# Kernel optimization log

Measured on AMD Instinct MI355X. Metric: run time of the kernel, lower is better.

The kernel has to match this reference:

```python
import jax, jax.numpy as jnp
import numpy as np

TREE_DEPTH = 4
N_LEAVES = 2 ** TREE_DEPTH      # 16
N_INTERNAL = 2 ** TREE_DEPTH - 1  # 15
TEMP = 1.0
EPS = 1e-5


def _build_paths(depth):
    nl = 2 ** depth
    pi = np.zeros((nl, depth), np.int32)
    pd = np.zeros((nl, depth), np.float32)
    for leaf in range(nl):
        node = 0
        for d in range(depth):
            pi[leaf, d] = node
            bit = (leaf >> (depth - 1 - d)) & 1
            pd[leaf, d] = 1.0 - bit
            node = 2 * node + 1 + bit
    return jnp.asarray(pi), jnp.asarray(pd)

PATH_IDX, PATH_DIR = _build_paths(TREE_DEPTH)


def setup_inputs() -> dict:
    key = jax.random.key(0)
    k0, k1, k2, k3 = jax.random.split(key, 4)
    B, S, D, O, T = 4, 2048, 1024, 512, 16
    x = jax.random.normal(k0, (B, S, D), jnp.float32)
    decision_weights = 0.1 * jax.random.normal(k1, (T, N_INTERNAL, D), jnp.float32)
    decision_biases = jnp.zeros((T, N_INTERNAL), jnp.float32)
    xavier = float(np.sqrt(2.0 / (N_LEAVES + O)))
    leaf_outputs = xavier * jax.random.normal(k2, (T, N_LEAVES, O), jnp.float32)
    gate_w = 0.02 * jax.random.normal(k3, (D, T), jnp.float32)
    gate_b = jnp.zeros((T,), jnp.float32)
    node_temp_logits = jnp.zeros((T, N_INTERNAL), jnp.float32)
    ln_gamma = jnp.ones((O,), jnp.float32)
    ln_beta = jnp.zeros((O,), jnp.float32)
    return dict(x=x, decision_weights=decision_weights, decision_biases=decision_biases,
                leaf_outputs=leaf_outputs, gate_w=gate_w, gate_b=gate_b,
                node_temp_logits=node_temp_logits, ln_gamma=ln_gamma, ln_beta=ln_beta)


def reference(x, decision_weights, decision_biases, leaf_outputs,
              gate_w, gate_b, node_temp_logits, ln_gamma, ln_beta):
    # decision logits: (B,S,T,N)
    logits = jnp.einsum('bsd,tnd->bstn', x, decision_weights) + decision_biases
    # per-node learnable temperature (softplus(0.5413) ~= 1)
    node_temps = TEMP * jax.nn.softplus(node_temp_logits + 0.5413)
    decisions = jax.nn.sigmoid(logits / node_temps)
    # gather decisions along each root->leaf path: (B,S,T,L,depth)
    relevant = decisions[..., PATH_IDX]
    probs_per_level = PATH_DIR * relevant + (1.0 - PATH_DIR) * (1.0 - relevant)
    leaf_probs = jnp.prod(probs_per_level, axis=-1)  # (B,S,T,L)
    per_tree = jnp.einsum('bstl,tlo->bsto', leaf_probs, leaf_outputs)
    gate = jax.nn.softmax(x @ gate_w + gate_b, axis=-1)  # (B,S,T)
    out = jnp.einsum('bsto,bst->bso', per_tree, gate)
    # LayerNorm over last dim
    mu = jnp.mean(out, axis=-1, keepdims=True)
    var = jnp.var(out, axis=-1, keepdims=True)
    return (out - mu) / jnp.sqrt(var + EPS) * ln_gamma + ln_beta
```

## Files before the change

kernel.cpp:

```cpp
#include <hip/hip_runtime.h>
#include <math.h>

#define TOK 8192
#define DD  1024
#define OO  512
#define NC  256

#define WC4_HI 0
#define WC4_LO (512*1024)
#define LO4_HI (1024*1024)
#define LO4_LO (1280*1024)
#define PAR_B  (1536*1024)

typedef __attribute__((ext_vector_type(8))) short short8;
typedef __attribute__((ext_vector_type(4))) float f32x4;

#define MFMA16(a,b,c) __builtin_amdgcn_mfma_f32_16x16x32_bf16((a),(b),(c),0,0,0)

__device__ __forceinline__ ushort f2bh(float f) {
  union { float f; unsigned u; } v; v.f = f;
  unsigned r = v.u + 0x7fffu + ((v.u >> 16) & 1u);
  return (ushort)(r >> 16);
}
__device__ __forceinline__ float bh2f(ushort h) {
  union { unsigned u; float f; } v; v.u = ((unsigned)h) << 16; return v.f;
}
__device__ __forceinline__ void split2(float f, ushort& h, ushort& l) {
  h = f2bh(f);
  l = f2bh(f - bh2f(h));
}

__global__ __launch_bounds__(256) void k_prep(
    const float* __restrict__ dw, const float* __restrict__ db,
    const float* __restrict__ lo_in, const float* __restrict__ gw,
    const float* __restrict__ ntl, char* __restrict__ ws) {
  const int bid = blockIdx.x, tid = threadIdx.x;
  if (bid < 16) {
    __shared__ char pt[65536];
    const int n0 = (bid & 3) * 64;
    const int k0 = (bid >> 2) * 256;
    const int kl4 = (tid & 63) << 2;
#pragma unroll
    for (int i = 0; i < 16; ++i) {
      const int row = (tid >> 6) + 4 * i;
      const int n = n0 + row;
      float v[4];
      if (n < 240) {
        const float4 t4 = *(const float4*)&dw[(size_t)n * DD + k0 + kl4];
        v[0] = t4.x; v[1] = t4.y; v[2] = t4.z; v[3] = t4.w;
      } else {
        const int t = n - 240;
#pragma unroll
        for (int c = 0; c < 4; ++c) v[c] = gw[(size_t)(k0 + kl4 + c) * 16 + t];
      }
      ushort4 h, l;
      split2(v[0], h.x, l.x); split2(v[1], h.y, l.y);
      split2(v[2], h.z, l.z); split2(v[3], h.w, l.w);
      const int u = kl4 >> 3, half = (kl4 >> 2) & 1;
      const int boff = row * 512 + ((u ^ (row & 31)) << 4) + half * 8;
      *(ushort4*)(pt + boff) = h;
      *(ushort4*)(pt + 32768 + boff) = l;
    }
    __syncthreads();
#pragma unroll
    for (int j = 0; j < 8; ++j) {
      const int u = tid + 256 * j;
      const int c = u & 63;
      const int kk = u >> 6;
      const int src = c * 512 + ((kk ^ (c & 31)) << 4);
      const size_t dst = ((size_t)((k0 >> 3) + kk) * 256 + n0 + c) * 16;
      *(short8*)(ws + WC4_HI + dst) = *(const short8*)(pt + src);
      *(short8*)(ws + WC4_LO + dst) = *(const short8*)(pt + 32768 + src);
    }
  } else if (bid < 80) {
    const int idx  = (bid - 16) * 256 + tid;
    const int k8   = idx >> 9;
    const int ocol = idx & 511;
    float v[8];
#pragma unroll
    for (int c = 0; c < 8; ++c) v[c] = lo_in[(size_t)(k8 * 8 + c) * OO + ocol];
    short8 h, l;
#pragma unroll
    for (int e = 0; e < 8; ++e) {
      ushort hh, ll; split2(v[e], hh, ll);
      h[e] = (short)hh; l[e] = (short)ll;
    }
    const size_t o16 = ((size_t)k8 * 512 + ocol) * 16;
    *(short8*)(ws + LO4_HI + o16) = h;
    *(short8*)(ws + LO4_LO + o16) = l;
  } else {
    if (tid < 240) {
      float v = ntl[tid] + 0.5413f;
      float sp = (v > 20.f) ? v : log1pf(expf(v));
      float* par = (float*)(ws + PAR_B);
      par[tid]       = db[tid];
      par[240 + tid] = 1.0f / sp;
    }
  }
}

#define XSB(b)  ((b) * 16384)
#define WF_HI   32768
#define WF_LO   49152
#define SM_SZ   65536

__global__ __launch_bounds__(512) void k_fused(
    const float* __restrict__ x, const char* __restrict__ ws,
    const float* __restrict__ gate_b, const float* __restrict__ gamma,
    const float* __restrict__ beta, float* __restrict__ out) {
  __shared__ __align__(16) char sm[SM_SZ];

  const char* wc4_hi = ws + WC4_HI;
  const char* wc4_lo = ws + WC4_LO;
  const char* lo4_hi = ws + LO4_HI;
  const char* lo4_lo = ws + LO4_LO;
  const float* par   = (const float*)(ws + PAR_B);

  const int tid  = threadIdx.x;
  const int wv   = tid >> 6;
  const int lane = tid & 63;
  const int l15  = lane & 15;
  const int kgrp = lane >> 4;
  const int m0   = blockIdx.x * 32;

  f32x4 acc00 = {0,0,0,0}, acc01 = {0,0,0,0}, acc10 = {0,0,0,0}, acc11 = {0,0,0,0};
  short8 ah0, ah1, al0, al1;
  short8 b1h[4][2], b1l[4][2];
  float4 pxa, pxb;

  auto xload = [&](int CH) {
    const int m_ = tid >> 5, kl = (tid & 31) << 2;
    pxa = *(const float4*)&x[(size_t)(m0 + m_) * DD + CH * 128 + kl];
    pxb = *(const float4*)&x[(size_t)(m0 + 16 + m_) * DD + CH * 128 + kl];
  };
  auto xstore = [&](int BUF) {
    const int kl2 = ((tid & 31) << 2) * 2;
    ushort4 h, l;
    split2(pxa.x, h.x, l.x); split2(pxa.y, h.y, l.y);
    split2(pxa.z, h.z, l.z); split2(pxa.w, h.w, l.w);
    {
      const int m_ = tid >> 5;
      const int off = (m_ * 256 + kl2) ^ ((m_ & 15) << 4);
      *(ushort4*)(sm + XSB(BUF) + off) = h;
      *(ushort4*)(sm + XSB(BUF) + 8192 + off) = l;
    }
    split2(pxb.x, h.x, l.x); split2(pxb.y, h.y, l.y);
    split2(pxb.z, h.z, l.z); split2(pxb.w, h.w, l.w);
    {
      const int m_ = 16 + (tid >> 5);
      const int off = (m_ * 256 + kl2) ^ ((m_ & 15) << 4);
      *(ushort4*)(sm + XSB(BUF) + off) = h;
      *(ushort4*)(sm + XSB(BUF) + 8192 + off) = l;
    }
  };
#define LOADB1(F, S) do {                                               \
    const int Fc = (F) < 31 ? (F) : 31;                                 \
    const size_t base = ((size_t)(Fc * 4 + kgrp) * 256) * 16;           \
    _Pragma("unroll")                                                   \
    for (int j = 0; j < 2; ++j) {                                       \
      const size_t o = base + (size_t)(wv * 32 + j * 16 + l15) * 16;    \
      b1h[S][j] = *(const short8*)(wc4_hi + o);                         \
      b1l[S][j] = *(const short8*)(wc4_lo + o);                         \
    }                                                                   \
  } while (0)
  auto afrag = [&](int CB, int KS) {
    const int k0 = KS * 64 + kgrp * 16;
    const int a0 = (l15 * 256 + k0) ^ ((l15 & 15) << 4);
    const int a1 = ((16 + l15) * 256 + k0) ^ ((l15 & 15) << 4);
    ah0 = *(const short8*)(sm + XSB(CB) + a0);
    al0 = *(const short8*)(sm + XSB(CB) + 8192 + a0);
    ah1 = *(const short8*)(sm + XSB(CB) + a1);
    al1 = *(const short8*)(sm + XSB(CB) + 8192 + a1);
  };
#define MFMASTEP(S) do {                                                   \
    acc00 = MFMA16(ah0, b1h[S][0], acc00); acc00 = MFMA16(ah0, b1l[S][0], acc00); \
    acc00 = MFMA16(al0, b1h[S][0], acc00);                                 \
    acc01 = MFMA16(ah0, b1h[S][1], acc01); acc01 = MFMA16(ah0, b1l[S][1], acc01); \
    acc01 = MFMA16(al0, b1h[S][1], acc01);                                 \
    acc10 = MFMA16(ah1, b1h[S][0], acc10); acc10 = MFMA16(ah1, b1l[S][0], acc10); \
    acc10 = MFMA16(al1, b1h[S][0], acc10);                                 \
    acc11 = MFMA16(ah1, b1h[S][1], acc11); acc11 = MFMA16(ah1, b1l[S][1], acc11); \
    acc11 = MFMA16(al1, b1h[S][1], acc11);                                 \
  } while (0)

  xload(0);
  xstore(0);
  LOADB1(0, 0);
  LOADB1(1, 1);

  for (int ch = 0; ch < 8; ++ch) {
    __syncthreads();
    const int cb = ch & 1;
    if (ch < 7) xload(ch + 1);
    const int f = ch * 4;
    LOADB1(f + 2, 2); afrag(cb, 0); MFMASTEP(0);
    LOADB1(f + 3, 3); afrag(cb, 1); MFMASTEP(1);
    LOADB1(f + 4, 0); afrag(cb, 2); MFMASTEP(2);
    LOADB1(f + 5, 1); afrag(cb, 3); MFMASTEP(3);
    if (ch < 7) xstore(cb ^ 1);
  }
  __syncthreads();

  {
    float* actp = (float*)sm;
    const f32x4 a[2][2] = {{acc00, acc01}, {acc10, acc11}};
#pragma unroll
    for (int mi = 0; mi < 2; ++mi)
#pragma unroll
      for (int j = 0; j < 2; ++j)
#pragma unroll
        for (int r = 0; r < 4; ++r) {
          const int row = mi * 16 + kgrp * 4 + r;
          const int col = wv * 32 + j * 16 + l15;
          actp[row * 256 + col] = a[mi][j][r];
        }
  }
  __syncthreads();

  short8 c2h[3][4], c2l[3][4];
#define LOADB2(F, S) do {                                               \
    const size_t base = ((size_t)((F) * 4 + kgrp) * 512) * 16;          \
    _Pragma("unroll")                                                   \
    for (int t = 0; t < 4; ++t) {                                       \
      const size_t o = base + (size_t)(wv * 64 + t * 16 + l15) * 16;    \
      c2h[S][t] = *(const short8*)(lo4_hi + o);                         \
      c2l[S][t] = *(const short8*)(lo4_lo + o);                         \
    }                                                                   \
  } while (0)
  LOADB2(0, 0);

  {
    const float* actp = (const float*)sm;
    const int token = tid >> 4;
    const int tr    = tid & 15;
    const float* arow_p = actp + token * 256;

    float dec[15];
#pragma unroll
    for (int i = 0; i < 15; ++i) {
      const int ci = tr * 15 + i;
      const float z = (arow_p[ci] + par[ci]) * par[240 + ci];
      dec[i] = 1.f / (1.f + expf(-z));
    }
    float gl = arow_p[240 + tr] + gate_b[tr];
    float gmax = gl;
#pragma unroll
    for (int msk = 8; msk >= 1; msk >>= 1) gmax = fmaxf(gmax, __shfl_xor(gmax, msk, 16));
    const float ge = expf(gl - gmax);
    float gsum = ge;
#pragma unroll
    for (int msk = 8; msk >= 1; msk >>= 1) gsum += __shfl_xor(gsum, msk, 16);
    const float gate = ge / gsum;

    float lp[16];
#pragma unroll
    for (int l = 0; l < 16; ++l) {
      float p = gate;
      int node = 0;
#pragma unroll
      for (int d = 0; d < 4; ++d) {
        const int bit = (l >> (3 - d)) & 1;
        p *= bit ? (1.f - dec[node]) : dec[node];
        node = 2 * node + 1 + bit;
      }
      lp[l] = p;
    }
    short8 h0, h1, l0, l1;
#pragma unroll
    for (int e = 0; e < 8; ++e) {
      ushort hh, ll;
      split2(lp[e], hh, ll);     h0[e] = (short)hh; l0[e] = (short)ll;
      split2(lp[8 + e], hh, ll); h1[e] = (short)hh; l1[e] = (short)ll;
    }
    const int b0 = (token * 512 + tr * 32) ^ ((token & 15) << 4);
    const int b1 = (token * 512 + tr * 32 + 16) ^ ((token & 15) << 4);
    *(short8*)(sm + WF_HI + b0) = h0;
    *(short8*)(sm + WF_HI + b1) = h1;
    *(short8*)(sm + WF_LO + b0) = l0;
    *(short8*)(sm + WF_LO + b1) = l1;
  }
  __syncthreads();

  f32x4 ac0[4], ac1[4];
#pragma unroll
  for (int t = 0; t < 4; ++t) { ac0[t] = (f32x4){0,0,0,0}; ac1[t] = (f32x4){0,0,0,0}; }
  short8 wah0, wah1, wal0, wal1;
  auto wafrag = [&](int FC) {
    const int k0 = FC * 64 + kgrp * 16;
    const int a0 = (l15 * 512 + k0) ^ ((l15 & 15) << 4);
    const int a1 = ((16 + l15) * 512 + k0) ^ ((l15 & 15) << 4);
    wah0 = *(const short8*)(sm + WF_HI + a0);
    wal0 = *(const short8*)(sm + WF_LO + a0);
    wah1 = *(const short8*)(sm + WF_HI + a1);
    wal1 = *(const short8*)(sm + WF_LO + a1);
  };
#define MFMA2STEP(S) do {                                                  \
    _Pragma("unroll")                                                      \
    for (int t = 0; t < 4; ++t) {                                          \
      ac0[t] = MFMA16(wah0, c2h[S][t], ac0[t]);                            \
      ac0[t] = MFMA16(wah0, c2l[S][t], ac0[t]);                            \
      ac0[t] = MFMA16(wal0, c2h[S][t], ac0[t]);                            \
      ac1[t] = MFMA16(wah1, c2h[S][t], ac1[t]);                            \
      ac1[t] = MFMA16(wah1, c2l[S][t], ac1[t]);                            \
      ac1[t] = MFMA16(wal1, c2h[S][t], ac1[t]);                            \
    }                                                                      \
  } while (0)

  LOADB2(1, 1);
  LOADB2(2, 2); wafrag(0); MFMA2STEP(0);
  LOADB2(3, 0); wafrag(1); MFMA2STEP(1);
  LOADB2(4, 1); wafrag(2); MFMA2STEP(2);
  LOADB2(5, 2); wafrag(3); MFMA2STEP(0);
  LOADB2(6, 0); wafrag(4); MFMA2STEP(1);
  LOADB2(7, 1); wafrag(5); MFMA2STEP(2);
  wafrag(6); MFMA2STEP(0);
  wafrag(7); MFMA2STEP(1);

  float* ps = (float*)sm;
#pragma unroll
  for (int mi = 0; mi < 2; ++mi)
#pragma unroll
    for (int r = 0; r < 4; ++r) {
      float s = 0.f, q = 0.f;
#pragma unroll
      for (int t = 0; t < 4; ++t) {
        const float v = (mi == 0) ? ac0[t][r] : ac1[t][r];
        s += v; q += v * v;
      }
#pragma unroll
      for (int msk = 8; msk >= 1; msk >>= 1) {
        s += __shfl_xor(s, msk, 16);
        q += __shfl_xor(q, msk, 16);
      }
      if (l15 == 0) {
        const int row = mi * 16 + kgrp * 4 + r;
        ps[(row * 8 + wv) * 2 + 0] = s;
        ps[(row * 8 + wv) * 2 + 1] = q;
      }
    }
  __syncthreads();

#pragma unroll
  for (int mi = 0; mi < 2; ++mi)
#pragma unroll
    for (int r = 0; r < 4; ++r) {
      const int row = mi * 16 + kgrp * 4 + r;
      float S = 0.f, Q = 0.f;
#pragma unroll
      for (int p = 0; p < 8; ++p) {
        S += ps[(row * 8 + p) * 2 + 0];
        Q += ps[(row * 8 + p) * 2 + 1];
      }
      const float mu  = S * (1.f / 512.f);
      const float var = Q * (1.f / 512.f) - mu * mu;
      const float rs  = rsqrtf(var + 1e-5f);
#pragma unroll
      for (int t = 0; t < 4; ++t) {
        const int col = wv * 64 + t * 16 + l15;
        const float v = (mi == 0) ? ac0[t][r] : ac1[t][r];
        out[(size_t)(m0 + row) * OO + col] = (v - mu) * rs * gamma[col] + beta[col];
      }
    }
}

extern "C" void kernel_launch(void* const* d_in, const int* in_sizes, int n_in,
                              void* d_out, int out_size, void* d_ws, size_t ws_size,
                              hipStream_t stream) {
  const float* x   = (const float*)d_in[0];
  const float* dw  = (const float*)d_in[1];
  const float* db  = (const float*)d_in[2];
  const float* lo  = (const float*)d_in[3];
  const float* gw  = (const float*)d_in[4];
  const float* gb  = (const float*)d_in[5];
  const float* ntl = (const float*)d_in[6];
  const float* g   = (const float*)d_in[7];
  const float* b   = (const float*)d_in[8];
  char* ws   = (char*)d_ws;
  float* out = (float*)d_out;

  k_prep<<<81, 256, 0, stream>>>(dw, db, lo, gw, ntl, ws);
  k_fused<<<256, 512, 0, stream>>>(x, ws, gb, g, b, out);
}
```

Measured before the change: 124.3 us.

## Double block size to 1024 threads, splitting output columns across 16 waves

Raises the fused kernel's block from 512 to 1024 threads, so 16 waves each own half as many output columns in both GEMM stages. Per-thread accumulators, weight fragments and x loads are halved. The leaf-probability stage is restricted to the first 512 threads, and the LayerNorm partial reduction now spans 16 waves. The goal is more latency hiding per CU with only 256 blocks, at the cost of more A-fragment LDS reads per wave, an idle half-block in the decision stage, and tighter register limits under the 1024 launch bound.

```diff
diff --git a/kernel.cpp b/kernel.cpp
--- a/kernel.cpp
+++ b/kernel.cpp
@@ -104,7 +104,7 @@
 #define WF_LO   49152
 #define SM_SZ   65536
 
-__global__ __launch_bounds__(512) void k_fused(
+__global__ __launch_bounds__(1024) void k_fused(
     const float* __restrict__ x, const char* __restrict__ ws,
     const float* __restrict__ gate_b, const float* __restrict__ gamma,
     const float* __restrict__ beta, float* __restrict__ out) {
@@ -123,64 +123,47 @@
   const int kgrp = lane >> 4;
   const int m0   = blockIdx.x * 32;
 
-  f32x4 acc00 = {0,0,0,0}, acc01 = {0,0,0,0}, acc10 = {0,0,0,0}, acc11 = {0,0,0,0};
+  f32x4 acc00 = {0,0,0,0}, acc10 = {0,0,0,0};
   short8 ah0, ah1, al0, al1;
-  short8 b1h[4][2], b1l[4][2];
-  float4 pxa, pxb;
+  short8 b1h[4], b1l[4];
+  float4 px;
+
+  const int xm = tid >> 5;
+  const int xk = (tid & 31) << 2;
 
   auto xload = [&](int CH) {
-    const int m_ = tid >> 5, kl = (tid & 31) << 2;
-    pxa = *(const float4*)&x[(size_t)(m0 + m_) * DD + CH * 128 + kl];
-    pxb = *(const float4*)&x[(size_t)(m0 + 16 + m_) * DD + CH * 128 + kl];
+    px = *(const float4*)&x[(size_t)(m0 + xm) * DD + CH * 128 + xk];
   };
   auto xstore = [&](int BUF) {
-    const int kl2 = ((tid & 31) << 2) * 2;
     ushort4 h, l;
-    split2(pxa.x, h.x, l.x); split2(pxa.y, h.y, l.y);
-    split2(pxa.z, h.z, l.z); split2(pxa.w, h.w, l.w);
-    {
-      const int m_ = tid >> 5;
-      const int off = (m_ * 256 + kl2) ^ ((m_ & 15) << 4);
-      *(ushort4*)(sm + XSB(BUF) + off) = h;
-      *(ushort4*)(sm + XSB(BUF) + 8192 + off) = l;
-    }
-    split2(pxb.x, h.x, l.x); split2(pxb.y, h.y, l.y);
-    split2(pxb.z, h.z, l.z); split2(pxb.w, h.w, l.w);
-    {
-      const int m_ = 16 + (tid >> 5);
-      const int off = (m_ * 256 + kl2) ^ ((m_ & 15) << 4);
-      *(ushort4*)(sm + XSB(BUF) + off) = h;
-      *(ushort4*)(sm + XSB(BUF) + 8192 + off) = l;
-    }
+    split2(px.x, h.x, l.x); split2(px.y, h.y, l.y);
+    split2(px.z, h.z, l.z); split2(px.w, h.w, l.w);
+    const int off = (xm * 256 + xk * 2) ^ ((xm & 15) << 4);
+    *(ushort4*)(sm + XSB(BUF) + off) = h;
+    *(ushort4*)(sm + XSB(BUF) + 8192 + off) = l;
   };
 #define LOADB1(F, S) do {                                               \
     const int Fc = (F) < 31 ? (F) : 31;                                 \
-    const size_t base = ((size_t)(Fc * 4 + kgrp) * 256) * 16;           \
-    _Pragma("unroll")                                                   \
-    for (int j = 0; j < 2; ++j) {                                       \
-      const size_t o = base + (size_t)(wv * 32 + j * 16 + l15) * 16;    \
-      b1h[S][j] = *(const short8*)(wc4_hi + o);                         \
-      b1l[S][j] = *(const short8*)(wc4_lo + o);                         \
-    }                                                                   \
+    const size_t o = ((size_t)(Fc * 4 + kgrp) * 256 + wv * 16 + l15) * 16; \
+    b1h[S] = *(const short8*)(wc4_hi + o);                              \
+    b1l[S] = *(const short8*)(wc4_lo + o);                              \
   } while (0)
   auto afrag = [&](int CB, int KS) {
     const int k0 = KS * 64 + kgrp * 16;
-    const int a0 = (l15 * 256 + k0) ^ ((l15 & 15) << 4);
-    const int a1 = ((16 + l15) * 256 + k0) ^ ((l15 & 15) << 4);
+    const int a0 = (l15 * 256 + k0) ^ (l15 << 4);
+    const int a1 = ((16 + l15) * 256 + k0) ^ (l15 << 4);
     ah0 = *(const short8*)(sm + XSB(CB) + a0);
     al0 = *(const short8*)(sm + XSB(CB) + 8192 + a0);
     ah1 = *(const short8*)(sm + XSB(CB) + a1);
     al1 = *(const short8*)(sm + XSB(CB) + 8192 + a1);
   };
-#define MFMASTEP(S) do {                                                   \
-    acc00 = MFMA16(ah0, b1h[S][0], acc00); acc00 = MFMA16(ah0, b1l[S][0], acc00); \
-    acc00 = MFMA16(al0, b1h[S][0], acc00);                                 \
-    acc01 = MFMA16(ah0, b1h[S][1], acc01); acc01 = MFMA16(ah0, b1l[S][1], acc01); \
-    acc01 = MFMA16(al0, b1h[S][1], acc01);                                 \
-    acc10 = MFMA16(ah1, b1h[S][0], acc10); acc10 = MFMA16(ah1, b1l[S][0], acc10); \
-    acc10 = MFMA16(al1, b1h[S][0], acc10);                                 \
-    acc11 = MFMA16(ah1, b1h[S][1], acc11); acc11 = MFMA16(ah1, b1l[S][1], acc11); \
-    acc11 = MFMA16(al1, b1h[S][1], acc11);                                 \
+#define MFMASTEP(S) do {                                                \
+    acc00 = MFMA16(ah0, b1h[S], acc00);                                 \
+    acc00 = MFMA16(ah0, b1l[S], acc00);                                 \
+    acc00 = MFMA16(al0, b1h[S], acc00);                                 \
+    acc10 = MFMA16(ah1, b1h[S], acc10);                                 \
+    acc10 = MFMA16(ah1, b1l[S], acc10);                                 \
+    acc10 = MFMA16(al1, b1h[S], acc10);                                 \
   } while (0)
 
   xload(0);
@@ -203,33 +186,29 @@
 
   {
     float* actp = (float*)sm;
-    const f32x4 a[2][2] = {{acc00, acc01}, {acc10, acc11}};
-#pragma unroll
-    for (int mi = 0; mi < 2; ++mi)
-#pragma unroll
-      for (int j = 0; j < 2; ++j)
-#pragma unroll
-        for (int r = 0; r < 4; ++r) {
-          const int row = mi * 16 + kgrp * 4 + r;
-          const int col = wv * 32 + j * 16 + l15;
-          actp[row * 256 + col] = a[mi][j][r];
-        }
+    const int col = wv * 16 + l15;
+#pragma unroll
+    for (int r = 0; r < 4; ++r) {
+      actp[(kgrp * 4 + r) * 256 + col]      = acc00[r];
+      actp[(16 + kgrp * 4 + r) * 256 + col] = acc10[r];
+    }
   }
   __syncthreads();
 
-  short8 c2h[3][4], c2l[3][4];
+  short8 c2h[3][2], c2l[3][2];
 #define LOADB2(F, S) do {                                               \
     const size_t base = ((size_t)((F) * 4 + kgrp) * 512) * 16;          \
     _Pragma("unroll")                                                   \
-    for (int t = 0; t < 4; ++t) {                                       \
-      const size_t o = base + (size_t)(wv * 64 + t * 16 + l15) * 16;    \
+    for (int t = 0; t < 2; ++t) {                                       \
+      const size_t o = base + (size_t)(wv * 32 + t * 16 + l15) * 16;    \
       c2h[S][t] = *(const short8*)(lo4_hi + o);                         \
       c2l[S][t] = *(const short8*)(lo4_lo + o);                         \
     }                                                                   \
   } while (0)
   LOADB2(0, 0);
-
-  {
+  LOADB2(1, 1);
+
+  if (tid < 512) {
     const float* actp = (const float*)sm;
     const int token = tid >> 4;
     const int tr    = tid & 15;
@@ -281,32 +260,31 @@
   }
   __syncthreads();
 
-  f32x4 ac0[4], ac1[4];
-#pragma unroll
-  for (int t = 0; t < 4; ++t) { ac0[t] = (f32x4){0,0,0,0}; ac1[t] = (f32x4){0,0,0,0}; }
+  f32x4 ac0[2], ac1[2];
+#pragma unroll
+  for (int t = 0; t < 2; ++t) { ac0[t] = (f32x4){0,0,0,0}; ac1[t] = (f32x4){0,0,0,0}; }
   short8 wah0, wah1, wal0, wal1;
   auto wafrag = [&](int FC) {
     const int k0 = FC * 64 + kgrp * 16;
-    const int a0 = (l15 * 512 + k0) ^ ((l15 & 15) << 4);
-    const int a1 = ((16 + l15) * 512 + k0) ^ ((l15 & 15) << 4);
+    const int a0 = (l15 * 512 + k0) ^ (l15 << 4);
+    const int a1 = ((16 + l15) * 512 + k0) ^ (l15 << 4);
     wah0 = *(const short8*)(sm + WF_HI + a0);
     wal0 = *(const short8*)(sm + WF_LO + a0);
     wah1 = *(const short8*)(sm + WF_HI + a1);
     wal1 = *(const short8*)(sm + WF_LO + a1);
   };
-#define MFMA2STEP(S) do {                                                  \
-    _Pragma("unroll")                                                      \
-    for (int t = 0; t < 4; ++t) {                                          \
-      ac0[t] = MFMA16(wah0, c2h[S][t], ac0[t]);                            \
-      ac0[t] = MFMA16(wah0, c2l[S][t], ac0[t]);                            \
-      ac0[t] = MFMA16(wal0, c2h[S][t], ac0[t]);                            \
-      ac1[t] = MFMA16(wah1, c2h[S][t], ac1[t]);                            \
-      ac1[t] = MFMA16(wah1, c2l[S][t], ac1[t]);                            \
-      ac1[t] = MFMA16(wal1, c2h[S][t], ac1[t]);                            \
-    }                                                                      \
+#define MFMA2STEP(S) do {                                               \
+    _Pragma("unroll")                                                   \
+    for (int t = 0; t < 2; ++t) {                                       \
+      ac0[t] = MFMA16(wah0, c2h[S][t], ac0[t]);                         \
+      ac0[t] = MFMA16(wah0, c2l[S][t], ac0[t]);                         \
+      ac0[t] = MFMA16(wal0, c2h[S][t], ac0[t]);                         \
+      ac1[t] = MFMA16(wah1, c2h[S][t], ac1[t]);                         \
+      ac1[t] = MFMA16(wah1, c2l[S][t], ac1[t]);                         \
+      ac1[t] = MFMA16(wal1, c2h[S][t], ac1[t]);                         \
+    }                                                                   \
   } while (0)
 
-  LOADB2(1, 1);
   LOADB2(2, 2); wafrag(0); MFMA2STEP(0);
   LOADB2(3, 0); wafrag(1); MFMA2STEP(1);
   LOADB2(4, 1); wafrag(2); MFMA2STEP(2);
@@ -323,7 +301,7 @@
     for (int r = 0; r < 4; ++r) {
       float s = 0.f, q = 0.f;
 #pragma unroll
-      for (int t = 0; t < 4; ++t) {
+      for (int t = 0; t < 2; ++t) {
         const float v = (mi == 0) ? ac0[t][r] : ac1[t][r];
         s += v; q += v * v;
       }
@@ -334,8 +312,8 @@
       }
       if (l15 == 0) {
         const int row = mi * 16 + kgrp * 4 + r;
-        ps[(row * 8 + wv) * 2 + 0] = s;
-        ps[(row * 8 + wv) * 2 + 1] = q;
+        ps[(row * 16 + wv) * 2 + 0] = s;
+        ps[(row * 16 + wv) * 2 + 1] = q;
       }
     }
   __syncthreads();
@@ -347,16 +325,16 @@
       const int row = mi * 16 + kgrp * 4 + r;
       float S = 0.f, Q = 0.f;
 #pragma unroll
-      for (int p = 0; p < 8; ++p) {
-        S += ps[(row * 8 + p) * 2 + 0];
-        Q += ps[(row * 8 + p) * 2 + 1];
+      for (int p = 0; p < 16; ++p) {
+        S += ps[(row * 16 + p) * 2 + 0];
+        Q += ps[(row * 16 + p) * 2 + 1];
       }
       const float mu  = S * (1.f / 512.f);
       const float var = Q * (1.f / 512.f) - mu * mu;
       const float rs  = rsqrtf(var + 1e-5f);
 #pragma unroll
-      for (int t = 0; t < 4; ++t) {
-        const int col = wv * 64 + t * 16 + l15;
+      for (int t = 0; t < 2; ++t) {
+        const int col = wv * 32 + t * 16 + l15;
         const float v = (mi == 0) ? ac0[t][r] : ac1[t][r];
         out[(size_t)(m0 + row) * OO + col] = (v - mu) * rs * gamma[col] + beta[col];
       }
@@ -379,5 +357,5 @@
   float* out = (float*)d_out;
 
   k_prep<<<81, 256, 0, stream>>>(dw, db, lo, gw, ntl, ws);
-  k_fused<<<256, 512, 0, stream>>>(x, ws, gb, g, b, out);
-}
+  k_fused<<<256, 1024, 0, stream>>>(x, ws, gb, g, b, out);
+}
```

After: 124.1 us. About the same (-0.1%).
